# Kernel tuning notes

Measured on AMD Instinct MI355X. Metric: run time of the kernel, lower is better.

## Reference

```python
import jax, jax.numpy as jnp
import numpy as np

N, F_IN, HID, NCLS, E = 100000, 256, 256, 32, 3200000
NHEADS, HDIM, MFEAT = 4, 64, 266  # MFEAT = int(HDIM * ln(HDIM)), performer default
ALPHA, KSTEPS, EPS = 0.1, 10, 1e-4


def setup_inputs() -> dict:
    key = jax.random.key(0)
    ks = jax.random.split(key, 16)
    p = lambda k, sh: (jax.random.normal(k, sh, dtype=jnp.float32) * 0.02)
    return {
        "x": jax.random.normal(ks[0], (N, F_IN), dtype=jnp.float32),
        "edge_index": jax.random.randint(ks[1], (2, E), 0, N, dtype=jnp.int64),
        "lin1_w": p(ks[2], (HID, F_IN)), "lin1_b": p(ks[3], (HID,)),
        "lin2_w": p(ks[4], (NCLS, 2 * HID)), "lin2_b": p(ks[5], (NCLS,)),
        "q_w": p(ks[6], (HID, F_IN)), "q_b": p(ks[7], (HID,)),
        "k_w": p(ks[8], (HID, F_IN)), "k_b": p(ks[9], (HID,)),
        "v_w": p(ks[10], (HID, F_IN)), "v_b": p(ks[11], (HID,)),
        "proj": jax.random.normal(ks[12], (MFEAT, HDIM), dtype=jnp.float32),
    }


def _softmax_kernel(data, proj, is_query):
    # performer_pytorch softmax random-feature map
    d = data.shape[-1]
    m = proj.shape[0]
    dn = d ** -0.25
    ratio = m ** -0.5
    data_dash = jnp.einsum('bhnd,md->bhnm', data * dn, proj)
    diag = 0.5 * (dn ** 2) * jnp.sum(data * data, axis=-1, keepdims=True)  # [b,h,n,1]
    if is_query:
        mx = jax.lax.stop_gradient(jnp.max(data_dash, axis=-1, keepdims=True))
    else:
        mx = jax.lax.stop_gradient(jnp.max(data_dash, axis=(-2, -1), keepdims=True))
    return ratio * (jnp.exp(data_dash - diag - mx) + EPS)


def _fast_attention(q, k, v, proj):
    # non-causal performer linear attention; q,k,v: [b,h,n,d]
    qp = _softmax_kernel(q, proj, True)   # [b,h,n,m]
    kp = _softmax_kernel(k, proj, False)  # [b,h,n,m]
    k_sum = jnp.sum(kp, axis=-2)                                   # [b,h,m]
    d_inv = 1.0 / jnp.einsum('bhnm,bhm->bhn', qp, k_sum)           # [b,h,n]
    context = jnp.einsum('bhnm,bhnd->bhmd', kp, v)                 # [b,h,m,d]
    return jnp.einsum('bhmd,bhnm,bhn->bhnd', context, qp, d_inv)   # [b,h,n,d]


def _appnp(x, edge_index, n):
    # gcn_norm with self-loops, then K iterations of x <- (1-a) A_hat x + a h
    src = jnp.concatenate([edge_index[0], jnp.arange(n, dtype=edge_index.dtype)])
    dst = jnp.concatenate([edge_index[1], jnp.arange(n, dtype=edge_index.dtype)])
    deg = jax.ops.segment_sum(jnp.ones_like(dst, dtype=x.dtype), dst, num_segments=n)
    dis = jnp.where(deg > 0, jax.lax.rsqrt(deg), 0.0)
    w = (dis[src] * dis[dst])[:, None]  # [E+N, 1]
    h = x
    for _ in range(KSTEPS):
        msg = jax.ops.segment_sum(x[src] * w, dst, num_segments=n)
        x = (1.0 - ALPHA) * msg + ALPHA * h
    return x


def reference(x, edge_index, lin1_w, lin1_b, lin2_w, lin2_b,
              q_w, q_b, k_w, k_b, v_w, v_b, proj):
    n = x.shape[0]
    # dropout layers are identity in eval mode
    xu = x[None]  # [1, N, F]
    q = (xu @ q_w.T + q_b).reshape(1, n, NHEADS, HDIM).transpose(0, 2, 1, 3)
    k = (xu @ k_w.T + k_b).reshape(1, n, NHEADS, HDIM).transpose(0, 2, 1, 3)
    v = (xu @ v_w.T + v_b).reshape(1, n, NHEADS, HDIM).transpose(0, 2, 1, 3)
    attn = _fast_attention(q, k, v, proj)                      # [1,h,n,d]
    trans = attn.transpose(0, 2, 1, 3).reshape(n, HID)         # [N, HID]
    gnn1 = x @ lin1_w.T + lin1_b                               # [N, HID]
    cat = jax.nn.elu(jnp.concatenate([gnn1, trans], axis=1))   # [N, 2*HID]
    gnn2 = jax.nn.elu(cat @ lin2_w.T + lin2_b)                 # [N, NCLS]
    final = _appnp(gnn2, edge_index, n)
    return jax.nn.log_softmax(final, axis=1), final
```

## Files before the change

### kernel.cpp

```cpp
#include <hip/hip_runtime.h>
#include <hip/hip_fp16.h>

#define NH 4
#define HD 64
#define MF 266
#define MP 288
#define NB 192
#define NBQ 128
#define DN 0.35355339059327373f
#define RATIO 0.06131393394849658f
#define EPSRF 1e-4f
#define REPS (RATIO*EPSRF)

typedef unsigned short u16;
typedef unsigned int u32;
typedef __attribute__((ext_vector_type(8))) short bf16x8;
typedef __attribute__((ext_vector_type(4))) float f32x4;
#define MFMA16(a,b,c) __builtin_amdgcn_mfma_f32_16x16x32_bf16(a,b,c,0,0,0)

__device__ __forceinline__ float bf2f(u16 u){ return __uint_as_float(((u32)u)<<16); }
__device__ __forceinline__ u16 f2bf(float f){ u32 u = __float_as_uint(f); u += 0x7FFFu + ((u>>16)&1u); return (u16)(u>>16); }
__device__ __forceinline__ u32 pack2bf(float a, float b){ return ((u32)f2bf(b)<<16) | f2bf(a); }
__device__ __forceinline__ float eluf(float x){ return x>0.f ? x : (expf(x)-1.f); }

__global__ void k_cvtw(const float* __restrict__ qw, const float* __restrict__ kw,
                       const float* __restrict__ vw, const float* __restrict__ lw,
                       const float* __restrict__ l2w, const float* __restrict__ proj,
                       u16* __restrict__ Wb, u16* __restrict__ projp, u16* __restrict__ l2wb){
  int i = blockIdx.x*256 + threadIdx.x;
  if (i < 262144){
    int sec = i>>16, r = i&65535;
    const float* s = sec==0?qw : sec==1?kw : sec==2?vw : lw;
    Wb[i] = f2bf(s[r]);
  }
  if (i < MP*64){
    int r = i>>6, c = i&63;
    projp[i] = f2bf(r < MF ? proj[r*64 + c] : 0.f);
  }
  if (i < 32*512) l2wb[i] = f2bf(l2w[i]);
}

__global__ __launch_bounds__(512,6) void k_proj(
    const float* __restrict__ x, const u16* __restrict__ Wb,
    const float* __restrict__ qb, const float* __restrict__ kb,
    const float* __restrict__ vb, const float* __restrict__ lb,
    u16* __restrict__ Q, u16* __restrict__ K, u16* __restrict__ V,
    u16* __restrict__ G1, int n)
{
  __shared__ u32 Xs[64*128];
  const int tid = threadIdx.x;
  const int w = tid>>6, l = tid&63;
  const int wr = w>>2, wc = w&3;
  const int lm = l&15, lk = l>>4;
  const int row0 = blockIdx.x*64;
  #pragma unroll
  for (int q=0;q<8;++q){
    int idx = q*512 + tid;
    int r = idx>>6, c4 = idx&63;
    int rr = row0 + r; if (rr > n-1) rr = n-1;
    float4 v = *(const float4*)(x + (size_t)rr*256 + c4*4);
    int word = (c4*2) ^ ((r&7)<<2);
    *(uint2*)&Xs[r*128 + word] = make_uint2(pack2bf(v.x,v.y), pack2bf(v.z,v.w));
  }
  __syncthreads();
  #pragma unroll 1
  for (int ct=0; ct<8; ++ct){
    const int c0 = ct*128 + wc*32;
    f32x4 acc[2][2] = {};
    #pragma unroll 2
    for (int kt=0; kt<8; ++kt){
      bf16x8 Af[2], Bf[2];
      #pragma unroll
      for (int jj=0;jj<2;jj++)
        Bf[jj] = *(const bf16x8*)(Wb + (size_t)(c0 + jj*16 + lm)*256 + kt*32 + lk*8);
      #pragma unroll
      for (int i=0;i<2;i++){
        const int rl = wr*32 + i*16 + lm;
        Af[i] = *(const bf16x8*)&Xs[rl*128 + ((kt*16 + lk*4) ^ ((rl&7)<<2))];
      }
      #pragma unroll
      for (int i=0;i<2;i++)
        #pragma unroll
        for (int jj=0;jj<2;jj++)
          acc[i][jj] = MFMA16(Af[i], Bf[jj], acc[i][jj]);
    }
    const int sel = c0>>8;
    const float* bp = sel==0?qb : sel==1?kb : sel==2?vb : lb;
    u16* d3 = sel==0?Q : sel==1?K : sel==2?V : G1;
    u32* dst32 = (u32*)d3;
    const bool even = (lm&1)==0;
    #pragma unroll
    for (int jj=0;jj<2;jj++){
      const int cc = (c0&255) + jj*16 + lm;
      const float bias = bp[cc];
      const int ccA = cc & ~1;
      const int hh = ccA>>6, dd = ccA&63;
      #pragma unroll
      for (int i=0;i<2;i++){
        const int rb = row0 + wr*32 + i*16 + lk*4;
        u32 m01 = pack2bf(acc[i][jj][0]+bias, acc[i][jj][1]+bias);
        u32 m23 = pack2bf(acc[i][jj][2]+bias, acc[i][jj][3]+bias);
        u32 oa = __shfl_xor(m01,1);
        u32 ob = __shfl_xor(m23,1);
        u32 wA = even ? ((m01 & 0xffffu) | ((oa & 0xffffu)<<16))
                      : ((ob  & 0xffffu) | ((m23 & 0xffffu)<<16));
        u32 wB = even ? ((m01 >> 16) | (oa & 0xffff0000u))
                      : ((ob  >> 16) | (m23 & 0xffff0000u));
        const int rA = rb + (even ? 0 : 2);
        const int rB = rA + 1;
        if (sel==3){
          if (rA < n) dst32[(size_t)rA*128 + (ccA>>1)] = wA;
          if (rB < n) dst32[(size_t)rB*128 + (ccA>>1)] = wB;
        } else {
          if (rA < n) dst32[(((size_t)hh*n + rA)<<5) + (dd>>1)] = wA;
          if (rB < n) dst32[(((size_t)hh*n + rB)<<5) + (dd>>1)] = wB;
        }
      }
    }
  }
}

__global__ void k_vcs(const u16* __restrict__ Vb, float* __restrict__ vcs, int n){
  const int h = blockIdx.y, tid = threadIdx.x;
  const int d = tid&63, seg = tid>>6;
  float s = 0.f;
  for (int node = blockIdx.x*4 + seg; node < n; node += 256)
    s += bf2f(Vb[(((size_t)h*n + node)<<6) + d]);
  __shared__ float sm[4][64];
  sm[seg][d] = s; __syncthreads();
  if (tid < 64){
    float t2 = sm[0][tid]+sm[1][tid]+sm[2][tid]+sm[3][tid];
    atomicAdd(vcs + h*64 + tid, t2);
  }
}

__global__ __launch_bounds__(256) void k_ctx(
    const u16* __restrict__ Kb, const u16* __restrict__ Vb,
    const u16* __restrict__ projp,
    float* __restrict__ ctxp, float* __restrict__ ksump,
    u32* __restrict__ kmaxg, int n)
{
  __shared__ u32 kpT[288*32];
  __shared__ u16 Vt[64][72];
  __shared__ float redk[4][288];
  const int tid = threadIdx.x;
  const int w = tid>>6, l = tid&63;
  const int bb = blockIdx.x;
  const int h = blockIdx.y;
  const int lm = l&15, lk = l>>4;
  f32x4 cacc[18] = {};
  float ksa[18] = {};
  float mreg = -3.0e38f;
  const int ntile = (n+63)>>6;
  #pragma unroll 1
  for (int t=bb; t<ntile; t+=NB){
    const int n0 = t*64;
    __syncthreads();
    #pragma unroll
    for (int q=0;q<2;q++){
      int e8 = tid + q*256;
      int nn = e8>>3, d0 = (e8&7)*8;
      uint4 rv = make_uint4(0,0,0,0);
      if (n0+nn < n) rv = *(const uint4*)(Vb + (((size_t)h*n + n0+nn)<<6) + d0);
      const u16* pv = (const u16*)&rv;
      #pragma unroll
      for (int s=0;s<8;s++) Vt[d0+s][nn] = pv[s];
    }
    int rr = n0 + w*16 + lm; if (rr > n-1) rr = n-1;
    const u16* Kbase = Kb + (((size_t)h*n + rr)<<6);
    bf16x8 af0 = *(const bf16x8*)(Kbase + lk*8);
    bf16x8 af1 = *(const bf16x8*)(Kbase + 32 + lk*8);
    float dg = 0.f;
    #pragma unroll
    for (int i2=0;i2<8;i2++){
      float a = bf2f(((const u16*)&af0)[i2]);
      float b = bf2f(((const u16*)&af1)[i2]);
      dg += a*a + b*b;
    }
    dg += __shfl_xor(dg,16); dg += __shfl_xor(dg,32);
    dg *= 0.0625f;
    float dgr[4];
    #pragma unroll
    for (int j=0;j<4;j++) dgr[j] = __shfl(dg, lk*4+j, 16);
    #pragma unroll
    for (int mt=0; mt<18; ++mt){
      bf16x8 b0 = *(const bf16x8*)(projp + (size_t)(mt*16+lm)*64 + lk*8);
      bf16x8 b1 = *(const bf16x8*)(projp + (size_t)(mt*16+lm)*64 + 32 + lk*8);
      f32x4 D = {0,0,0,0};
      D = MFMA16(af0, b0, D);
      D = MFMA16(af1, b1, D);
      const int m = mt*16 + lm;
      const bool vm = m < MF;
      float colsum = 0.f;
      u32 pk0 = 0, pk1 = 0;
      #pragma unroll
      for (int j=0;j<4;j++){
        float ddash = DN * D[j];
        float kp = 0.f;
        if (vm && (n0 + w*16 + lk*4 + j) < n){
          kp = RATIO * __expf(ddash - dgr[j]);
          mreg = fmaxf(mreg, ddash);
          colsum += kp;
        }
        if (j<2) pk0 |= ((u32)f2bf(kp)) << (16*j);
        else     pk1 |= ((u32)f2bf(kp)) << (16*(j-2));
      }
      const int wn0 = w*8 + lk*2;
      *(uint2*)&kpT[m*32 + (wn0 ^ ((m&7)<<2))] = make_uint2(pk0, pk1);
      colsum += __shfl_xor(colsum,16); colsum += __shfl_xor(colsum,32);
      ksa[mt] += colsum;
    }
    __syncthreads();
    #pragma unroll
    for (int mt=0; mt<18; ++mt){
      const int m = mt*16 + lm;
      #pragma unroll
      for (int ks=0;ks<2;++ks){
        bf16x8 a = *(const bf16x8*)&kpT[m*32 + ((ks*16 + lk*4) ^ ((m&7)<<2))];
        bf16x8 bv = *(const bf16x8*)&Vt[w*16+lm][ks*32 + lk*8];
        cacc[mt] = MFMA16(a, bv, cacc[mt]);
      }
    }
  }
  float* cp = ctxp + ((size_t)(h*NB + bb))*MP*64;
  #pragma unroll
  for (int mt=0;mt<18;++mt){
    #pragma unroll
    for (int j=0;j<4;j++){
      int m = mt*16 + lk*4 + j;
      cp[(size_t)m*64 + w*16 + lm] = cacc[mt][j];
    }
  }
  if (l < 16){
    #pragma unroll
    for (int mt=0;mt<18;++mt) redk[w][mt*16+lm] = ksa[mt];
  }
  __shared__ float redm[4];
  float mr = mreg;
  #pragma unroll
  for (int s=1;s<64;s<<=1) mr = fmaxf(mr, __shfl_xor(mr, s));
  if (l==0) redm[w] = mr;
  __syncthreads();
  for (int m2=tid; m2<MP; m2+=256){
    float s = redk[0][m2]+redk[1][m2]+redk[2][m2]+redk[3][m2];
    ksump[((size_t)(h*NB+bb))*MP + m2] = s;
  }
  if (tid==0){
    float bm = fmaxf(fmaxf(redm[0],redm[1]), fmaxf(redm[2],redm[3]));
    u32 b = __float_as_uint(bm);
    u32 enc = (b & 0x80000000u) ? ~b : (b | 0x80000000u);
    atomicMax(kmaxg + h, enc);
  }
}

__global__ void k_reduce(const float* __restrict__ ctxp, const float* __restrict__ ksump,
                         const u32* __restrict__ kmaxg, const float* __restrict__ vcs,
                         u16* __restrict__ ctxT, float* __restrict__ ksum, int n)
{
  const int T1 = NH*MP*64;
  int idx = blockIdx.x*256 + threadIdx.x;
  if (idx < T1){
    int h = idx/(MP*64), r = idx - h*MP*64, m = r>>6, d = r&63;
    u32 ee = kmaxg[h]; u32 b = (ee & 0x80000000u) ? (ee ^ 0x80000000u) : ~ee;
    float sc = __expf(-__uint_as_float(b));
    float s = 0.f;
    for (int bb=0; bb<NB; ++bb) s += ctxp[(((size_t)(h*NB+bb))*MP + m)*64 + d];
    float val = (m < MF) ? (sc*s + REPS*vcs[h*64 + d]) : 0.f;
    ctxT[((size_t)h*64 + d)*MP + m] = f2bf(val);
  } else if (idx < T1 + NH*MP){
    int k2 = idx - T1, h = k2/MP, m = k2 - h*MP;
    u32 ee = kmaxg[h]; u32 b = (ee & 0x80000000u) ? (ee ^ 0x80000000u) : ~ee;
    float sc = __expf(-__uint_as_float(b));
    float s = 0.f;
    for (int bb=0; bb<NB; ++bb) s += ksump[((size_t)(h*NB+bb))*MP + m];
    ksum[h*MP + m] = (m < MF) ? (sc*s + REPS*(float)n) : 0.f;
  }
}

__global__ __launch_bounds__(256) void k_qattn(
    const u16* __restrict__ Qb, const u16* __restrict__ projp,
    const u16* __restrict__ ctxT, const float* __restrict__ ksum,
    u16* __restrict__ trans, int n)
{
  __shared__ u32 pj[288*32];
  __shared__ u16 qp_lds[4][16][168];
  const int tid = threadIdx.x;
  const int w = tid>>6, l = tid&63;
  const int h = blockIdx.y;
  const int lm = l&15, lk = l>>4;
  #pragma unroll
  for (int q=0; q<9; ++q){
    int cix = q*256 + tid;
    int row = cix>>3, c4 = (cix&7)*4;
    uint4 v = *(const uint4*)(projp + row*64 + c4*2);
    *(uint4*)&pj[row*32 + (c4 ^ ((row&7)<<2))] = v;
  }
  float ksm[18];
  #pragma unroll
  for (int mt=0;mt<18;++mt) ksm[mt] = ksum[h*MP + mt*16 + lm];
  __syncthreads();
  const int ntile = (n+63)>>6;
  #pragma unroll 1
  for (int t = blockIdx.x; t < ntile; t += NBQ){
    const int nb = t*64 + w*16;
    int rr = nb + lm; if (rr > n-1) rr = n-1;
    const u16* Qbase = Qb + (((size_t)h*n + rr)<<6);
    bf16x8 af0 = *(const bf16x8*)(Qbase + lk*8);
    bf16x8 af1 = *(const bf16x8*)(Qbase + 32 + lk*8);
    float dg = 0.f;
    #pragma unroll
    for (int i2=0;i2<8;i2++){
      float a = bf2f(((const u16*)&af0)[i2]);
      float b = bf2f(((const u16*)&af1)[i2]);
      dg += a*a + b*b;
    }
    dg += __shfl_xor(dg,16); dg += __shfl_xor(dg,32);
    dg *= 0.0625f;
    float dgr[4];
    #pragma unroll
    for (int j=0;j<4;j++) dgr[j] = __shfl(dg, lk*4+j, 16);
    f32x4 D[18];
    #pragma unroll
    for (int mt=0;mt<18;++mt){
      const int m = mt*16 + lm;
      bf16x8 b0 = *(const bf16x8*)&pj[m*32 + ((lk*4) ^ ((m&7)<<2))];
      bf16x8 b1 = *(const bf16x8*)&pj[m*32 + ((16 + lk*4) ^ ((m&7)<<2))];
      f32x4 z = {0,0,0,0};
      z = MFMA16(af0, b0, z);
      z = MFMA16(af1, b1, z);
      D[mt] = z;
    }
    float rmax[4] = {-3.0e38f,-3.0e38f,-3.0e38f,-3.0e38f};
    #pragma unroll
    for (int mt=0;mt<17;++mt){
      const bool vm = (mt<16) || (lm<10);
      #pragma unroll
      for (int j=0;j<4;j++){
        float dd = DN*D[mt][j];
        if (vm) rmax[j] = fmaxf(rmax[j], dd);
      }
    }
    #pragma unroll
    for (int j=0;j<4;j++){
      #pragma unroll
      for (int s=1;s<16;s<<=1) rmax[j] = fmaxf(rmax[j], __shfl_xor(rmax[j], s));
    }
    float den[4] = {0,0,0,0};
    f32x4 o[4] = {{0,0,0,0},{0,0,0,0},{0,0,0,0},{0,0,0,0}};
    #pragma unroll
    for (int mt=0;mt<10;++mt){
      #pragma unroll
      for (int j=0;j<4;j++){
        float qp = RATIO*(__expf(DN*D[mt][j] - dgr[j] - rmax[j]) + EPSRF);
        den[j] += qp * ksm[mt];
        qp_lds[w][lk*4+j][mt*16+lm] = f2bf(qp);
      }
    }
    #pragma unroll
    for (int ks=0;ks<5;++ks){
      bf16x8 av = *(const bf16x8*)&qp_lds[w][lm][ks*32 + lk*8];
      #pragma unroll
      for (int dt=0;dt<4;++dt){
        bf16x8 bv = *(const bf16x8*)(ctxT + (size_t)(h*64 + dt*16 + lm)*MP + ks*32 + lk*8);
        o[dt] = MFMA16(av, bv, o[dt]);
      }
    }
    #pragma unroll
    for (int mt=10;mt<18;++mt){
      #pragma unroll
      for (int j=0;j<4;j++){
        float qp = RATIO*(__expf(DN*D[mt][j] - dgr[j] - rmax[j]) + EPSRF);
        den[j] += qp * ksm[mt];
        qp_lds[w][lk*4+j][(mt-10)*16+lm] = f2bf(qp);
      }
    }
    #pragma unroll
    for (int ks=5;ks<9;++ks){
      bf16x8 av = *(const bf16x8*)&qp_lds[w][lm][(ks-5)*32 + lk*8];
      #pragma unroll
      for (int dt=0;dt<4;++dt){
        bf16x8 bv = *(const bf16x8*)(ctxT + (size_t)(h*64 + dt*16 + lm)*MP + ks*32 + lk*8);
        o[dt] = MFMA16(av, bv, o[dt]);
      }
    }
    #pragma unroll
    for (int j=0;j<4;j++){
      #pragma unroll
      for (int s=1;s<16;s<<=1) den[j] += __shfl_xor(den[j], s);
    }
    #pragma unroll
    for (int j=0;j<4;j++){
      const int node = nb + lk*4 + j;
      if (node < n){
        const float dv = 1.f/den[j];
        #pragma unroll
        for (int dt=0;dt<4;++dt)
          trans[(size_t)node*256 + h*64 + dt*16 + lm] = f2bf(o[dt][j]*dv);
      }
    }
  }
}

__global__ __launch_bounds__(256) void k_gnn2(
    const u16* __restrict__ G1, const u16* __restrict__ trans,
    const u16* __restrict__ l2wb, const float* __restrict__ l2b,
    u16* __restrict__ xb0, int n)
{
  __shared__ u32 cat[64*256];
  const int tid = threadIdx.x;
  const int w = tid>>6, l = tid&63;
  const int lm = l&15, lk = l>>4;
  const int n0 = blockIdx.x*64;
  #pragma unroll
  for (int src=0; src<2; ++src){
    const u16* S = src ? trans : G1;
    #pragma unroll
    for (int q=0;q<8;++q){
      int idx = q*256 + tid;
      int row = idx>>5, v8 = idx&31;
      int rr = n0+row; if (rr > n-1) rr = n-1;
      uint4 raw = *(const uint4*)(S + (size_t)rr*256 + v8*8);
      const u16* p = (const u16*)&raw;
      u32 o2[4];
      #pragma unroll
      for (int t2=0;t2<4;++t2)
        o2[t2] = pack2bf(eluf(bf2f(p[t2*2])), eluf(bf2f(p[t2*2+1])));
      int word = (v8*4 + src*128) ^ ((row&7)<<2);
      *(uint4*)&cat[row*256 + word] = *(uint4*)o2;
    }
  }
  __syncthreads();
  f32x4 acc[2] = {{0,0,0,0},{0,0,0,0}};
  const int rowl = w*16 + lm;
  #pragma unroll 4
  for (int kt=0; kt<16; ++kt){
    bf16x8 a = *(const bf16x8*)&cat[rowl*256 + ((kt*16 + lk*4) ^ ((rowl&7)<<2))];
    #pragma unroll
    for (int jj=0;jj<2;++jj){
      bf16x8 b = *(const bf16x8*)(l2wb + (size_t)(jj*16+lm)*512 + kt*32 + lk*8);
      acc[jj] = MFMA16(a, b, acc[jj]);
    }
  }
  #pragma unroll
  for (int jj=0;jj<2;++jj){
    const int o = jj*16 + lm;
    const float bias = l2b[o];
    #pragma unroll
    for (int jr=0;jr<4;++jr){
      const int node = n0 + w*16 + lk*4 + jr;
      if (node < n)
        xb0[(size_t)node*32 + o] = f2bf(eluf(acc[jj][jr] + bias));
    }
  }
}

__global__ void k_edgemode(const int* __restrict__ ei, int* __restrict__ mode){
  __shared__ int any;
  if (threadIdx.x==0) any = 0;
  __syncthreads();
  if (ei[threadIdx.x*2+1] != 0) any = 1;
  __syncthreads();
  if (threadIdx.x==0) *mode = any;
}
__device__ __forceinline__ int edge_at(const int* ei, int mode, size_t idx){
  if (mode) return ei[idx];
  return (int)((const long long*)ei)[idx];
}

__global__ void k_hist(const int* __restrict__ ei, const int* __restrict__ mode,
                       u32* __restrict__ deg, int e){
  const int md = *mode;
  for (size_t i = (size_t)blockIdx.x*blockDim.x + threadIdx.x; i < (size_t)e; i += (size_t)gridDim.x*blockDim.x)
    atomicAdd(&deg[edge_at(ei, md, (size_t)e + i)], 1u);
}
__global__ void k_dis(const u32* __restrict__ deg, float* __restrict__ dis, int n){
  int i = blockIdx.x*256 + threadIdx.x;
  if (i<n) dis[i] = rsqrtf((float)(deg[i] + 1u));
}
__global__ __launch_bounds__(1024) void k_scan(const u32* __restrict__ deg, u32* __restrict__ rowp, int n){
  __shared__ u32 wsum[16];
  __shared__ u32 carry;
  const int tid = threadIdx.x, lane = tid&63, wv = tid>>6;
  if (tid==0){ carry = 0u; rowp[0] = 0u; }
  __syncthreads();
  for (int base=0; base<n; base+=1024){
    int i = base + tid;
    u32 v = (i<n)? deg[i] : 0u;
    u32 s = v;
    #pragma unroll
    for (int off=1; off<64; off<<=1){
      u32 t = __shfl_up(s, off, 64);
      if (lane >= off) s += t;
    }
    if (lane==63) wsum[wv] = s;
    __syncthreads();
    if (wv==0){
      u32 ws = (lane<16)? wsum[lane] : 0u;
      #pragma unroll
      for (int off=1; off<16; off<<=1){
        u32 t = __shfl_up(ws, off, 64);
        if (lane >= off) ws += t;
      }
      if (lane<16) wsum[lane] = ws;
    }
    __syncthreads();
    u32 pre = carry + (wv ? wsum[wv-1] : 0u);
    if (i<n) rowp[i+1] = pre + s;
    __syncthreads();
    if (tid==0) carry += wsum[15];
    __syncthreads();
  }
}
__global__ void k_copy(const u32* __restrict__ a, u32* __restrict__ b, int n){
  int i = blockIdx.x*256 + threadIdx.x; if (i<n) b[i]=a[i];
}
__global__ void k_fill(const int* __restrict__ ei, const int* __restrict__ mode,
                       const float* __restrict__ dis,
                       u32* __restrict__ cur, uint2* __restrict__ cw, int e){
  const int md = *mode;
  for (size_t i = (size_t)blockIdx.x*blockDim.x + threadIdx.x; i < (size_t)e; i += (size_t)gridDim.x*blockDim.x){
    int s = edge_at(ei, md, i);
    int t = edge_at(ei, md, (size_t)e + i);
    u32 pos = atomicAdd(&cur[t], 1u);
    cw[pos] = make_uint2((u32)s, __float_as_uint(dis[s]*dis[t]));
  }
}

__global__ __launch_bounds__(256) void k_appnp(
    const u16* __restrict__ xin, const u16* __restrict__ hb16,
    u16* __restrict__ xout, const u32* __restrict__ rowp,
    const uint2* __restrict__ cw, const float* __restrict__ dis, int n)
{
  const int g = threadIdx.x>>3, j4 = threadIdx.x&7;
  const int node = blockIdx.x*32 + g;
  if (node >= n) return;
  const uint2* x64 = (const uint2*)xin;
  float d0 = dis[node];
  float dd = d0*d0;
  uint2 xv = x64[((size_t)node<<3) + j4];
  float a0 = dd*bf2f((u16)xv.x), a1 = dd*bf2f((u16)(xv.x>>16));
  float a2 = dd*bf2f((u16)xv.y), a3 = dd*bf2f((u16)(xv.y>>16));
  u32 r0 = rowp[node], r1 = rowp[node+1];
  u32 k = r0;
  for (; k+4 <= r1; k += 4){
    uint2 e0 = cw[k], e1 = cw[k+1], e2 = cw[k+2], e3 = cw[k+3];
    uint2 v0 = x64[((size_t)e0.x<<3)+j4], v1 = x64[((size_t)e1.x<<3)+j4];
    uint2 v2 = x64[((size_t)e2.x<<3)+j4], v3 = x64[((size_t)e3.x<<3)+j4];
    float w0=__uint_as_float(e0.y), w1=__uint_as_float(e1.y);
    float w2=__uint_as_float(e2.y), w3=__uint_as_float(e3.y);
    a0 += w0*bf2f((u16)v0.x) + w1*bf2f((u16)v1.x) + w2*bf2f((u16)v2.x) + w3*bf2f((u16)v3.x);
    a1 += w0*bf2f((u16)(v0.x>>16)) + w1*bf2f((u16)(v1.x>>16)) + w2*bf2f((u16)(v2.x>>16)) + w3*bf2f((u16)(v3.x>>16));
    a2 += w0*bf2f((u16)v0.y) + w1*bf2f((u16)v1.y) + w2*bf2f((u16)v2.y) + w3*bf2f((u16)v3.y);
    a3 += w0*bf2f((u16)(v0.y>>16)) + w1*bf2f((u16)(v1.y>>16)) + w2*bf2f((u16)(v2.y>>16)) + w3*bf2f((u16)(v3.y>>16));
  }
  for (; k < r1; ++k){
    uint2 e = cw[k];
    uint2 v = x64[((size_t)e.x<<3)+j4];
    float wgt = __uint_as_float(e.y);
    a0 += wgt*bf2f((u16)v.x);
    a1 += wgt*bf2f((u16)(v.x>>16));
    a2 += wgt*bf2f((u16)v.y);
    a3 += wgt*bf2f((u16)(v.y>>16));
  }
  uint2 hv = ((const uint2*)hb16)[((size_t)node<<3) + j4];
  uint2 o;
  o.x = pack2bf(0.9f*a0 + 0.1f*bf2f((u16)hv.x), 0.9f*a1 + 0.1f*bf2f((u16)(hv.x>>16)));
  o.y = pack2bf(0.9f*a2 + 0.1f*bf2f((u16)hv.y), 0.9f*a3 + 0.1f*bf2f((u16)(hv.y>>16)));
  ((uint2*)xout)[((size_t)node<<3) + j4] = o;
}

__global__ __launch_bounds__(256) void k_appnp_lsm(
    const u16* __restrict__ xin, const u16* __restrict__ hb16,
    float* __restrict__ out, const u32* __restrict__ rowp,
    const uint2* __restrict__ cw, const float* __restrict__ dis, int n)
{
  const int g = threadIdx.x>>3, j4 = threadIdx.x&7;
  const int node = blockIdx.x*32 + g;
  if (node >= n) return;
  const uint2* x64 = (const uint2*)xin;
  float d0 = dis[node];
  float dd = d0*d0;
  uint2 xv = x64[((size_t)node<<3) + j4];
  float a0 = dd*bf2f((u16)xv.x), a1 = dd*bf2f((u16)(xv.x>>16));
  float a2 = dd*bf2f((u16)xv.y), a3 = dd*bf2f((u16)(xv.y>>16));
  u32 r0 = rowp[node], r1 = rowp[node+1];
  u32 k = r0;
  for (; k+4 <= r1; k += 4){
    uint2 e0 = cw[k], e1 = cw[k+1], e2 = cw[k+2], e3 = cw[k+3];
    uint2 v0 = x64[((size_t)e0.x<<3)+j4], v1 = x64[((size_t)e1.x<<3)+j4];
    uint2 v2 = x64[((size_t)e2.x<<3)+j4], v3 = x64[((size_t)e3.x<<3)+j4];
    float w0=__uint_as_float(e0.y), w1=__uint_as_float(e1.y);
    float w2=__uint_as_float(e2.y), w3=__uint_as_float(e3.y);
    a0 += w0*bf2f((u16)v0.x) + w1*bf2f((u16)v1.x) + w2*bf2f((u16)v2.x) + w3*bf2f((u16)v3.x);
    a1 += w0*bf2f((u16)(v0.x>>16)) + w1*bf2f((u16)(v1.x>>16)) + w2*bf2f((u16)(v2.x>>16)) + w3*bf2f((u16)(v3.x>>16));
    a2 += w0*bf2f((u16)v0.y) + w1*bf2f((u16)v1.y) + w2*bf2f((u16)v2.y) + w3*bf2f((u16)v3.y);
    a3 += w0*bf2f((u16)(v0.y>>16)) + w1*bf2f((u16)(v1.y>>16)) + w2*bf2f((u16)(v2.y>>16)) + w3*bf2f((u16)(v3.y>>16));
  }
  for (; k < r1; ++k){
    uint2 e = cw[k];
    uint2 v = x64[((size_t)e.x<<3)+j4];
    float wgt = __uint_as_float(e.y);
    a0 += wgt*bf2f((u16)v.x);
    a1 += wgt*bf2f((u16)(v.x>>16));
    a2 += wgt*bf2f((u16)v.y);
    a3 += wgt*bf2f((u16)(v.y>>16));
  }
  uint2 hv = ((const uint2*)hb16)[((size_t)node<<3) + j4];
  float v0 = 0.9f*a0 + 0.1f*bf2f((u16)hv.x);
  float v1 = 0.9f*a1 + 0.1f*bf2f((u16)(hv.x>>16));
  float v2 = 0.9f*a2 + 0.1f*bf2f((u16)hv.y);
  float v3 = 0.9f*a3 + 0.1f*bf2f((u16)(hv.y>>16));
  float m = fmaxf(fmaxf(v0,v1), fmaxf(v2,v3));
  #pragma unroll
  for (int o2=1;o2<8;o2<<=1) m = fmaxf(m, __shfl_xor(m, o2, 8));
  float s = __expf(v0-m)+__expf(v1-m)+__expf(v2-m)+__expf(v3-m);
  #pragma unroll
  for (int o2=1;o2<8;o2<<=1) s += __shfl_xor(s, o2, 8);
  float ls = m + logf(s);
  float4 lsv = make_float4(v0-ls, v1-ls, v2-ls, v3-ls);
  *(float4*)(out + (size_t)node*32 + j4*4) = lsv;
  float4 raw = make_float4(v0, v1, v2, v3);
  *(float4*)(out + (size_t)n*32 + (size_t)node*32 + j4*4) = raw;
}

extern "C" void kernel_launch(void* const* d_in, const int* in_sizes, int n_in,
                              void* d_out, int out_size, void* d_ws, size_t ws_size,
                              hipStream_t stream)
{
  const float* x   = (const float*)d_in[0];
  const int*   ei  = (const int*)  d_in[1];
  const float* l1w = (const float*)d_in[2];
  const float* l1b = (const float*)d_in[3];
  const float* l2w = (const float*)d_in[4];
  const float* l2b = (const float*)d_in[5];
  const float* qw  = (const float*)d_in[6];
  const float* qb  = (const float*)d_in[7];
  const float* kw  = (const float*)d_in[8];
  const float* kb  = (const float*)d_in[9];
  const float* vw  = (const float*)d_in[10];
  const float* vb  = (const float*)d_in[11];
  const float* proj= (const float*)d_in[12];
  const int n = in_sizes[0] / 256;
  const int e = in_sizes[1] / 2;

  char* ws = (char*)d_ws;
  auto au = [](size_t v){ return (v + 255) & ~(size_t)255; };
  const size_t bQ = (size_t)n * 512;
  const size_t oQ = 0;
  const size_t oK = au(oQ + bQ);
  const size_t oV = au(oK + bQ);
  const size_t oG1 = au(oV + bQ);
  const size_t oCtxp = au(oG1 + bQ);
  const size_t bCtxp = (size_t)NH*NB*MP*64*4;
  const size_t oKsump = au(oCtxp + bCtxp);
  const size_t bKsump = (size_t)NH*NB*MP*4;
  const size_t oCtxT = au(oKsump + bKsump);
  const size_t oKsum = au(oCtxT + (size_t)NH*64*MP*2);
  const size_t oKmax = au(oKsum + (size_t)NH*MP*4);
  const size_t oVcs  = oKmax + 256;
  const size_t oMode = oVcs + 1024;
  const size_t oL2wb = au(oMode + 256);
  const size_t oWb   = au(oL2wb + 32768);
  const size_t oProjp= au(oWb + (size_t)1024*256*2);
  const size_t oTrans = oK;
  const size_t oG2 = oQ;
  const size_t oXb0 = au(oG2 + (size_t)n*32*4);
  const size_t oXbA = au(oXb0 + (size_t)n*32*2);
  const size_t oXbB = au(oXbA + (size_t)n*32*2);
  const size_t oDeg = au(oXbB + (size_t)n*32*2);
  const size_t oDis = au(oDeg + (size_t)n*4);
  const size_t oRowp= au(oDis + (size_t)n*4);
  const size_t oCur = au(oRowp + (size_t)(n+1)*4);
  const size_t oCw  = oV;
  (void)ws_size; (void)n_in; (void)out_size;

  u16* Q  = (u16*)(ws + oQ);
  u16* Kb = (u16*)(ws + oK);
  u16* Vb = (u16*)(ws + oV);
  u16* G1 = (u16*)(ws + oG1);
  float* ctxp = (float*)(ws + oCtxp);
  float* ksump= (float*)(ws + oKsump);
  u16*  ctxT  = (u16*)(ws + oCtxT);
  float* ksum = (float*)(ws + oKsum);
  u32*  kmax  = (u32*)(ws + oKmax);
  float* Vcs  = (float*)(ws + oVcs);
  int*  mode  = (int*)(ws + oMode);
  u16*  l2wb  = (u16*)(ws + oL2wb);
  u16*  Wb    = (u16*)(ws + oWb);
  u16*  projp = (u16*)(ws + oProjp);
  u16* trans  = (u16*)(ws + oTrans);
  u16* xb0    = (u16*)(ws + oXb0);
  u16* xbA    = (u16*)(ws + oXbA);
  u16* xbB    = (u16*)(ws + oXbB);
  u32* deg    = (u32*)(ws + oDeg);
  float* dis  = (float*)(ws + oDis);
  u32* rowp   = (u32*)(ws + oRowp);
  u32* cur    = (u32*)(ws + oCur);
  uint2* cw   = (uint2*)(ws + oCw);

  k_cvtw<<<1024,256,0,stream>>>(qw,kw,vw,l1w,l2w,proj,Wb,projp,l2wb);
  k_proj<<<(n+63)/64,512,0,stream>>>(x,Wb,qb,kb,vb,l1b,Q,Kb,Vb,G1,n);
  hipMemsetAsync(ws + oKmax, 0, 16, stream);
  hipMemsetAsync(ws + oVcs, 0, 1024, stream);
  k_vcs<<<dim3(64,4),256,0,stream>>>(Vb,Vcs,n);
  k_ctx<<<dim3(NB,NH),256,0,stream>>>(Kb,Vb,projp,ctxp,ksump,kmax,n);
  {
    int tot = NH*MP*64 + NH*MP;
    k_reduce<<<(tot+255)/256,256,0,stream>>>(ctxp,ksump,kmax,Vcs,ctxT,ksum,n);
  }
  k_qattn<<<dim3(NBQ,4),256,0,stream>>>(Q,projp,ctxT,ksum,trans,n);
  k_gnn2<<<(n+63)/64,256,0,stream>>>(G1,trans,l2wb,l2b,xb0,n);
  k_edgemode<<<1,256,0,stream>>>(ei,mode);
  hipMemsetAsync(ws + oDeg, 0, (size_t)n*4, stream);
  k_hist<<<2048,256,0,stream>>>(ei,mode,deg,e);
  k_dis<<<(n+255)/256,256,0,stream>>>(deg,dis,n);
  k_scan<<<1,1024,0,stream>>>(deg,rowp,n);
  k_copy<<<(n+255)/256,256,0,stream>>>(rowp,cur,n);
  k_fill<<<2048,256,0,stream>>>(ei,mode,dis,cur,cw,e);
  const u16* curx = xb0;
  u16* bufs[2] = {xbA, xbB};
  for (int it=0; it<9; ++it){
    u16* nxt = bufs[it&1];
    k_appnp<<<(n+31)/32,256,0,stream>>>(curx,xb0,nxt,rowp,cw,dis,n);
    curx = nxt;
  }
  k_appnp_lsm<<<(n+31)/32,256,0,stream>>>(curx,xb0,(float*)d_out,rowp,cw,dis,n);
}
```

Before: 1.576 ms.

## Enlarge projection row tile to 128 and swap MFMA operands for vectorized stores

The projection GEMM kernel now handles 128 rows per block instead of 64, doubling the shared X tile. Each weight fragment read from global memory is therefore reused across twice as many rows. The MFMA operands are swapped so weights act as A and X rows as B. This puts four consecutive output columns in each lane, so the epilogue loads bias as a float4 and writes 8-byte packed stores directly, dropping the shuffle-based pairing. The cost is 64KB of LDS per block and a lower occupancy hint (4 instead of 6), which may reduce latency hiding.

```diff
diff --git a/kernel.cpp b/kernel.cpp
--- a/kernel.cpp
+++ b/kernel.cpp
@@ -40,21 +40,21 @@
   if (i < 32*512) l2wb[i] = f2bf(l2w[i]);
 }
 
-__global__ __launch_bounds__(512,6) void k_proj(
+__global__ __launch_bounds__(512,4) void k_proj(
     const float* __restrict__ x, const u16* __restrict__ Wb,
     const float* __restrict__ qb, const float* __restrict__ kb,
     const float* __restrict__ vb, const float* __restrict__ lb,
     u16* __restrict__ Q, u16* __restrict__ K, u16* __restrict__ V,
     u16* __restrict__ G1, int n)
 {
-  __shared__ u32 Xs[64*128];
+  __shared__ u32 Xs[128*128];
   const int tid = threadIdx.x;
   const int w = tid>>6, l = tid&63;
   const int wr = w>>2, wc = w&3;
   const int lm = l&15, lk = l>>4;
-  const int row0 = blockIdx.x*64;
-  #pragma unroll
-  for (int q=0;q<8;++q){
+  const int row0 = blockIdx.x*128;
+  #pragma unroll 4
+  for (int q=0;q<16;++q){
     int idx = q*512 + tid;
     int r = idx>>6, c4 = idx&63;
     int rr = row0 + r; if (rr > n-1) rr = n-1;
@@ -66,54 +66,41 @@
   #pragma unroll 1
   for (int ct=0; ct<8; ++ct){
     const int c0 = ct*128 + wc*32;
-    f32x4 acc[2][2] = {};
+    f32x4 acc[2][4] = {};
     #pragma unroll 2
     for (int kt=0; kt<8; ++kt){
-      bf16x8 Af[2], Bf[2];
-      #pragma unroll
-      for (int jj=0;jj<2;jj++)
-        Bf[jj] = *(const bf16x8*)(Wb + (size_t)(c0 + jj*16 + lm)*256 + kt*32 + lk*8);
-      #pragma unroll
-      for (int i=0;i<2;i++){
-        const int rl = wr*32 + i*16 + lm;
-        Af[i] = *(const bf16x8*)&Xs[rl*128 + ((kt*16 + lk*4) ^ ((rl&7)<<2))];
+      bf16x8 Af[2], Bf[4];
+      #pragma unroll
+      for (int i=0;i<2;i++)
+        Af[i] = *(const bf16x8*)(Wb + (size_t)(c0 + i*16 + lm)*256 + kt*32 + lk*8);
+      #pragma unroll
+      for (int jj=0;jj<4;jj++){
+        const int rl = wr*64 + jj*16 + lm;
+        Bf[jj] = *(const bf16x8*)&Xs[rl*128 + ((kt*16 + lk*4) ^ ((rl&7)<<2))];
       }
       #pragma unroll
       for (int i=0;i<2;i++)
         #pragma unroll
-        for (int jj=0;jj<2;jj++)
+        for (int jj=0;jj<4;jj++)
           acc[i][jj] = MFMA16(Af[i], Bf[jj], acc[i][jj]);
     }
     const int sel = c0>>8;
     const float* bp = sel==0?qb : sel==1?kb : sel==2?vb : lb;
     u16* d3 = sel==0?Q : sel==1?K : sel==2?V : G1;
-    u32* dst32 = (u32*)d3;
-    const bool even = (lm&1)==0;
-    #pragma unroll
-    for (int jj=0;jj<2;jj++){
-      const int cc = (c0&255) + jj*16 + lm;
-      const float bias = bp[cc];
-      const int ccA = cc & ~1;
-      const int hh = ccA>>6, dd = ccA&63;
-      #pragma unroll
-      for (int i=0;i<2;i++){
-        const int rb = row0 + wr*32 + i*16 + lk*4;
-        u32 m01 = pack2bf(acc[i][jj][0]+bias, acc[i][jj][1]+bias);
-        u32 m23 = pack2bf(acc[i][jj][2]+bias, acc[i][jj][3]+bias);
-        u32 oa = __shfl_xor(m01,1);
-        u32 ob = __shfl_xor(m23,1);
-        u32 wA = even ? ((m01 & 0xffffu) | ((oa & 0xffffu)<<16))
-                      : ((ob  & 0xffffu) | ((m23 & 0xffffu)<<16));
-        u32 wB = even ? ((m01 >> 16) | (oa & 0xffff0000u))
-                      : ((ob  >> 16) | (m23 & 0xffff0000u));
-        const int rA = rb + (even ? 0 : 2);
-        const int rB = rA + 1;
-        if (sel==3){
-          if (rA < n) dst32[(size_t)rA*128 + (ccA>>1)] = wA;
-          if (rB < n) dst32[(size_t)rB*128 + (ccA>>1)] = wB;
-        } else {
-          if (rA < n) dst32[(((size_t)hh*n + rA)<<5) + (dd>>1)] = wA;
-          if (rB < n) dst32[(((size_t)hh*n + rB)<<5) + (dd>>1)] = wB;
+    #pragma unroll
+    for (int i=0;i<2;i++){
+      const int ccb = (c0&255) + i*16 + lk*4;
+      const float4 b4 = *(const float4*)(bp + ccb);
+      const int hh = ccb>>6, dd = ccb&63;
+      #pragma unroll
+      for (int jj=0;jj<4;jj++){
+        const int node = row0 + wr*64 + jj*16 + lm;
+        if (node < n){
+          uint2 o;
+          o.x = pack2bf(acc[i][jj][0]+b4.x, acc[i][jj][1]+b4.y);
+          o.y = pack2bf(acc[i][jj][2]+b4.z, acc[i][jj][3]+b4.w);
+          if (sel==3) *(uint2*)(d3 + (size_t)node*256 + ccb) = o;
+          else        *(uint2*)(d3 + (((size_t)hh*n + node)<<6) + dd) = o;
         }
       }
     }
@@ -699,7 +686,7 @@
   uint2* cw   = (uint2*)(ws + oCw);
 
   k_cvtw<<<1024,256,0,stream>>>(qw,kw,vw,l1w,l2w,proj,Wb,projp,l2wb);
-  k_proj<<<(n+63)/64,512,0,stream>>>(x,Wb,qb,kb,vb,l1b,Q,Kb,Vb,G1,n);
+  k_proj<<<(n+127)/128,512,0,stream>>>(x,Wb,qb,kb,vb,l1b,Q,Kb,Vb,G1,n);
   hipMemsetAsync(ws + oKmax, 0, 16, stream);
   hipMemsetAsync(ws + oVcs, 0, 1024, stream);
   k_vcs<<<dim3(64,4),256,0,stream>>>(Vb,Vcs,n);
```

New measurement: 1.538 ms (median of 2 runs). 1.02x faster.

## Sort nodes by degree within windows for APPNP balance; enlarge projection row tile

Applied to the files above, without the earlier changes.

A new kernel builds a permutation that orders nodes by in-degree inside each 256-node window, so each block of the APPNP propagation kernels handles groups of similar degree. This is meant to reduce lane divergence among the 8-thread node groups in a wave and give each wave a more even load. Separately, the projection GEMM now handles 128 rows per block instead of 64, with 4 row fragments per wave. That reuses each weight fragment over more rows, at the cost of more LDS and registers and lower occupancy. For n not divisible by 256, padded perm entries hold values at or above n and are skipped, though the tail window may write slots beyond n that fall inside its workspace allocation.

```diff
diff --git a/kernel.cpp b/kernel.cpp
--- a/kernel.cpp
+++ b/kernel.cpp
@@ -40,21 +40,21 @@
   if (i < 32*512) l2wb[i] = f2bf(l2w[i]);
 }
 
-__global__ __launch_bounds__(512,6) void k_proj(
+__global__ __launch_bounds__(512,4) void k_proj(
     const float* __restrict__ x, const u16* __restrict__ Wb,
     const float* __restrict__ qb, const float* __restrict__ kb,
     const float* __restrict__ vb, const float* __restrict__ lb,
     u16* __restrict__ Q, u16* __restrict__ K, u16* __restrict__ V,
     u16* __restrict__ G1, int n)
 {
-  __shared__ u32 Xs[64*128];
+  __shared__ u32 Xs[128*128];
   const int tid = threadIdx.x;
   const int w = tid>>6, l = tid&63;
   const int wr = w>>2, wc = w&3;
   const int lm = l&15, lk = l>>4;
-  const int row0 = blockIdx.x*64;
-  #pragma unroll
-  for (int q=0;q<8;++q){
+  const int row0 = blockIdx.x*128;
+  #pragma unroll 4
+  for (int q=0;q<16;++q){
     int idx = q*512 + tid;
     int r = idx>>6, c4 = idx&63;
     int rr = row0 + r; if (rr > n-1) rr = n-1;
@@ -66,20 +66,20 @@
   #pragma unroll 1
   for (int ct=0; ct<8; ++ct){
     const int c0 = ct*128 + wc*32;
-    f32x4 acc[2][2] = {};
+    f32x4 acc[4][2] = {};
     #pragma unroll 2
     for (int kt=0; kt<8; ++kt){
-      bf16x8 Af[2], Bf[2];
+      bf16x8 Af[4], Bf[2];
       #pragma unroll
       for (int jj=0;jj<2;jj++)
         Bf[jj] = *(const bf16x8*)(Wb + (size_t)(c0 + jj*16 + lm)*256 + kt*32 + lk*8);
       #pragma unroll
-      for (int i=0;i<2;i++){
-        const int rl = wr*32 + i*16 + lm;
+      for (int i=0;i<4;i++){
+        const int rl = wr*64 + i*16 + lm;
         Af[i] = *(const bf16x8*)&Xs[rl*128 + ((kt*16 + lk*4) ^ ((rl&7)<<2))];
       }
       #pragma unroll
-      for (int i=0;i<2;i++)
+      for (int i=0;i<4;i++)
         #pragma unroll
         for (int jj=0;jj<2;jj++)
           acc[i][jj] = MFMA16(Af[i], Bf[jj], acc[i][jj]);
@@ -96,8 +96,8 @@
       const int ccA = cc & ~1;
       const int hh = ccA>>6, dd = ccA&63;
       #pragma unroll
-      for (int i=0;i<2;i++){
-        const int rb = row0 + wr*32 + i*16 + lk*4;
+      for (int i=0;i<4;i++){
+        const int rb = row0 + wr*64 + i*16 + lk*4;
         u32 m01 = pack2bf(acc[i][jj][0]+bias, acc[i][jj][1]+bias);
         u32 m23 = pack2bf(acc[i][jj][2]+bias, acc[i][jj][3]+bias);
         u32 oa = __shfl_xor(m01,1);
@@ -526,13 +526,47 @@
   }
 }
 
+__global__ __launch_bounds__(256) void k_dperm(const u32* __restrict__ rowp,
+                                               u32* __restrict__ perm, int n){
+  __shared__ u32 keys[256];
+  __shared__ u32 hist[256];
+  __shared__ u32 scn[256];
+  const int tid = threadIdx.x;
+  const int base = blockIdx.x*256;
+  const int node = base + tid;
+  u32 key = 255u;
+  if (node < n){
+    u32 d = rowp[node+1] - rowp[node];
+    key = d > 254u ? 254u : d;
+  }
+  keys[tid] = key;
+  hist[tid] = 0u;
+  __syncthreads();
+  atomicAdd(&hist[key], 1u);
+  __syncthreads();
+  u32 sv = hist[tid];
+  scn[tid] = sv;
+  __syncthreads();
+  for (int off=1; off<256; off<<=1){
+    u32 t = (tid>=off)? scn[tid-off] : 0u;
+    __syncthreads();
+    scn[tid] += t;
+    __syncthreads();
+  }
+  u32 r = 0;
+  for (int j=0;j<tid;++j) if (keys[j]==key) ++r;
+  u32 pos = scn[key] - hist[key] + r;
+  perm[base + pos] = (u32)node;
+}
+
 __global__ __launch_bounds__(256) void k_appnp(
     const u16* __restrict__ xin, const u16* __restrict__ hb16,
     u16* __restrict__ xout, const u32* __restrict__ rowp,
-    const uint2* __restrict__ cw, const float* __restrict__ dis, int n)
+    const uint2* __restrict__ cw, const float* __restrict__ dis,
+    const u32* __restrict__ perm, int n)
 {
   const int g = threadIdx.x>>3, j4 = threadIdx.x&7;
-  const int node = blockIdx.x*32 + g;
+  const int node = (int)perm[blockIdx.x*32 + g];
   if (node >= n) return;
   const uint2* x64 = (const uint2*)xin;
   float d0 = dis[node];
@@ -572,10 +606,11 @@
 __global__ __launch_bounds__(256) void k_appnp_lsm(
     const u16* __restrict__ xin, const u16* __restrict__ hb16,
     float* __restrict__ out, const u32* __restrict__ rowp,
-    const uint2* __restrict__ cw, const float* __restrict__ dis, int n)
+    const uint2* __restrict__ cw, const float* __restrict__ dis,
+    const u32* __restrict__ perm, int n)
 {
   const int g = threadIdx.x>>3, j4 = threadIdx.x&7;
-  const int node = blockIdx.x*32 + g;
+  const int node = (int)perm[blockIdx.x*32 + g];
   if (node >= n) return;
   const uint2* x64 = (const uint2*)xin;
   float d0 = dis[node];
@@ -671,6 +706,8 @@
   const size_t oDis = au(oDeg + (size_t)n*4);
   const size_t oRowp= au(oDis + (size_t)n*4);
   const size_t oCur = au(oRowp + (size_t)(n+1)*4);
+  const int nwin = (n+255)/256;
+  const size_t oPerm= au(oCur + (size_t)(n+1)*4);
   const size_t oCw  = oV;
   (void)ws_size; (void)n_in; (void)out_size;
 
@@ -696,10 +733,11 @@
   float* dis  = (float*)(ws + oDis);
   u32* rowp   = (u32*)(ws + oRowp);
   u32* cur    = (u32*)(ws + oCur);
+  u32* perm   = (u32*)(ws + oPerm);
   uint2* cw   = (uint2*)(ws + oCw);
 
   k_cvtw<<<1024,256,0,stream>>>(qw,kw,vw,l1w,l2w,proj,Wb,projp,l2wb);
-  k_proj<<<(n+63)/64,512,0,stream>>>(x,Wb,qb,kb,vb,l1b,Q,Kb,Vb,G1,n);
+  k_proj<<<(n+127)/128,512,0,stream>>>(x,Wb,qb,kb,vb,l1b,Q,Kb,Vb,G1,n);
   hipMemsetAsync(ws + oKmax, 0, 16, stream);
   hipMemsetAsync(ws + oVcs, 0, 1024, stream);
   k_vcs<<<dim3(64,4),256,0,stream>>>(Vb,Vcs,n);
@@ -717,12 +755,13 @@
   k_scan<<<1,1024,0,stream>>>(deg,rowp,n);
   k_copy<<<(n+255)/256,256,0,stream>>>(rowp,cur,n);
   k_fill<<<2048,256,0,stream>>>(ei,mode,dis,cur,cw,e);
+  k_dperm<<<nwin,256,0,stream>>>(rowp,perm,n);
   const u16* curx = xb0;
   u16* bufs[2] = {xbA, xbB};
   for (int it=0; it<9; ++it){
     u16* nxt = bufs[it&1];
-    k_appnp<<<(n+31)/32,256,0,stream>>>(curx,xb0,nxt,rowp,cw,dis,n);
+    k_appnp<<<(n+31)/32,256,0,stream>>>(curx,xb0,nxt,rowp,cw,dis,perm,n);
     curx = nxt;
   }
-  k_appnp_lsm<<<(n+31)/32,256,0,stream>>>(curx,xb0,(float*)d_out,rowp,cw,dis,n);
-}
+  k_appnp_lsm<<<(n+31)/32,256,0,stream>>>(curx,xb0,(float*)d_out,rowp,cw,dis,perm,n);
+}
```

New measurement: 1.574 ms. Within noise of the previous version (-0.1%).
